# Optimization experiments

Measured on AMD Instinct MI355X. Metric: run time of the kernel, lower is better.

## Reference

```python
import jax, jax.numpy as jnp
import numpy as np

B, N, E = 64, 512, 262144
D_EMB = 128   # 2 * embedding_dim
D_H = 128     # residue_emb_dim == iegmn_lay_hid_dim
L = 5         # iegmn_n_lays
X_INIT = 0.25 # residual mix toward original coords (IEGMN x_connection_init)


def silu(x):
    return x * jax.nn.sigmoid(x)


def _edges(k):
    # within-graph random edges: pick a graph, then a node inside it
    g = jax.random.randint(k, (E,), 0, B)
    n = jax.random.randint(jax.random.fold_in(k, 1), (E,), 0, N)
    return (g * N + n).astype(jnp.int32)


def setup_inputs() -> dict:
    key = jax.random.key(0)
    ks = jax.random.split(key, 16)
    Nt = B * N
    s = 0.05
    feat = jax.random.normal(ks[0], (Nt, D_EMB), jnp.float32)
    coords = jax.random.normal(ks[1], (Nt, 3), jnp.float32)
    c_valid = (jax.random.uniform(ks[2], (B, N)) > 0.3).astype(jnp.float32)
    c_valid = c_valid.at[:, 0].set(1.0)  # avoid empty graphs
    return {
        'feat': feat,
        'coords': coords,
        'c_valid': c_valid,
        'edge_src': _edges(ks[3]), 'edge_dst': _edges(ks[4]),
        'cross_src': _edges(ks[5]), 'cross_dst': _edges(ks[6]),
        'W_emb': jax.random.normal(ks[7], (D_H, D_EMB), jnp.float32) * s,
        'We1': jax.random.normal(ks[8], (L, 2 * D_H + 1, D_H), jnp.float32) * s,
        'be1': jnp.zeros((L, D_H), jnp.float32),
        'We2': jax.random.normal(ks[9], (L, D_H, D_H), jnp.float32) * s,
        'be2': jnp.zeros((L, D_H), jnp.float32),
        'Wx': jax.random.normal(ks[10], (L, D_H, 1), jnp.float32) * s,
        'Wh': jax.random.normal(ks[11], (L, 3 * D_H, D_H), jnp.float32) * s,
        'bh': jnp.zeros((L, D_H), jnp.float32),
        'Wfc': jax.random.normal(ks[12], (3, D_H, D_H), jnp.float32) * s,
        'bfc': jnp.zeros((3, D_H), jnp.float32),
        'Wout': jax.random.normal(ks[13], (D_H, 1), jnp.float32) * s,
        'bout': jnp.zeros((1,), jnp.float32),
    }


def _deg_inv(dst, n):
    deg = jax.ops.segment_sum(jnp.ones(dst.shape[0], jnp.float32), dst, num_segments=n)
    return (1.0 / jnp.maximum(deg, 1.0))[:, None]


def _iegmn_layer(p, src, dst, x, h, x0, h0, deg_inv):
    We1, be1, We2, be2, Wx, Wh, bh = p
    n = x.shape[0]
    dx = x[src] - x[dst]                                  # [E, 3]
    d2 = jnp.sum(dx * dx, -1, keepdims=True)              # [E, 1]
    m = silu(jnp.concatenate([h[src], h[dst], d2], -1) @ We1 + be1)
    m = silu(m @ We2 + be2)                               # [E, D_H]
    coef = jnp.tanh(m @ Wx)                               # [E, 1]
    agg_x = jax.ops.segment_sum(dx * coef, dst, num_segments=n) * deg_inv
    x_new = X_INIT * x0 + (1.0 - X_INIT) * x + agg_x
    agg_m = jax.ops.segment_sum(m, dst, num_segments=n) * deg_inv
    h_new = silu(jnp.concatenate([h, agg_m, h0], -1) @ Wh + bh)
    return x_new, h_new


def reference(feat, coords, c_valid, edge_src, edge_dst, cross_src, cross_dst,
              W_emb, We1, be1, We2, be2, Wx, Wh, bh, Wfc, bfc, Wout, bout):
    Nt = feat.shape[0]
    h = feat @ W_emb.T          # embede (no bias)
    h0, x0, x = h, coords, coords
    dgi = _deg_inv(edge_dst, Nt)
    dci = _deg_inv(cross_dst, Nt)
    for k in range(L):
        p = tuple(t[k] for t in (We1, be1, We2, be2, Wx, Wh, bh))
        # branch == 'both': run layer on graph then cross_graph with same input h
        x, c1 = _iegmn_layer(p, edge_src, edge_dst, x, h, x0, h0, dgi)
        x, c2 = _iegmn_layer(p, cross_src, cross_dst, x, h, x0, h0, dci)
        h = c2 - c1             # dropout is identity at inference
    # masked sum-pool / count
    hb = h.reshape(B, N, D_H)
    pooled = jnp.sum(hb * c_valid[..., None], axis=1) / jnp.sum(c_valid, axis=1, keepdims=True)
    z = pooled
    for i in range(Wfc.shape[0]):
        z = jax.nn.relu(z @ Wfc[i] + bfc[i])
    out = jax.nn.sigmoid(z @ Wout + bout)
    return out.reshape(-1)      # [B]
```

## Files before the change

### kernel.cpp

```cpp
#include <hip/hip_runtime.h>

#define DEVINL __device__ __forceinline__

constexpr int NT   = 32768;
constexpr int DH   = 128;
constexpr int NE   = 262144;
constexpr int BGR  = 64;
constexpr int NPG  = 512;
constexpr int LAYS = 5;

typedef __attribute__((ext_vector_type(8))) short bf16x8;
typedef __attribute__((ext_vector_type(4))) float f32x4;
typedef __attribute__((ext_vector_type(4))) unsigned int uint4v;
typedef unsigned int uint;

DEVINL float siluf(float v){ return v * (1.0f/(1.0f + __expf(-v))); }
DEVINL float tanh_fast(float x){ float e = __expf(2.0f*x); return 1.0f - 2.0f/(e + 1.0f); }

DEVINL uint bf16_rne(float f){
  uint x = __float_as_uint(f);
  return (x + 0x7fffu + ((x>>16)&1u)) >> 16;
}

DEVINL void split8(const float* m, bf16x8& h, bf16x8& l){
  #pragma unroll
  for (int j=0;j<8;j++){
    uint x  = __float_as_uint(m[j]);
    uint hb = x >> 16;
    float hf = __uint_as_float(hb<<16);
    uint lb = bf16_rne(m[j] - hf);
    h[j] = (short)hb; l[j] = (short)lb;
  }
}

DEVINL f32x4 mma3(bf16x8 ah, bf16x8 al, bf16x8 bh, bf16x8 bl, f32x4 acc){
  acc = __builtin_amdgcn_mfma_f32_16x16x32_bf16(al, bh, acc, 0,0,0);
  acc = __builtin_amdgcn_mfma_f32_16x16x32_bf16(ah, bl, acc, 0,0,0);
  acc = __builtin_amdgcn_mfma_f32_16x16x32_bf16(ah, bh, acc, 0,0,0);
  return acc;
}

template<int TRANS>
__global__ __launch_bounds__(256) void k_prep(const float* __restrict__ src, short* __restrict__ dst){
  const int idx = blockIdx.x*256 + threadIdx.x;
  const int k = idx>>7, col = idx&127;
  const float v = TRANS ? src[(size_t)col*128 + k] : src[(size_t)k*128 + col];
  uint hb = __float_as_uint(v) >> 16;
  float hf = __uint_as_float(hb<<16);
  uint lb = bf16_rne(v - hf);
  const int kc = k>>5, q = (k&31)>>3, j = k&7;
  const size_t o = (size_t)kc*8192 + q*1024 + col*8 + j;
  dst[o]        = (short)hb;
  dst[o + 4096] = (short)lb;
}

__global__ __launch_bounds__(256) void k_hist(const int* __restrict__ dst, int* __restrict__ cnt){
  int e = blockIdx.x*256 + threadIdx.x;
  atomicAdd(&cnt[dst[e]], 1);
}

__global__ __launch_bounds__(1024) void k_scan(const int* __restrict__ cnt, int* __restrict__ cur){
  __shared__ int part[1024];
  const int tid = threadIdx.x;
  const int base = tid*32;
  int s = 0;
  for (int i=0;i<32;i++) s += cnt[base+i];
  const int own = s;
  part[tid] = s; __syncthreads();
  for (int off=1; off<1024; off<<=1){
    int v = (tid>=off) ? part[tid-off] : 0;
    __syncthreads();
    part[tid] += v;
    __syncthreads();
  }
  int run = part[tid] - own;
  for (int i=0;i<32;i++){ cur[base+i] = run; run += cnt[base+i]; }
}

__global__ __launch_bounds__(256) void k_invdeg(const int* __restrict__ cnt, float* __restrict__ dinv){
  int n = blockIdx.x*256 + threadIdx.x;
  int c = cnt[n];
  dinv[n] = 1.0f / (float)(c > 1 ? c : 1);
}

__global__ __launch_bounds__(256) void k_scatter(const int* __restrict__ dst, int* __restrict__ cur,
                                                 int* __restrict__ perm){
  int e = blockIdx.x*256 + threadIdx.x;
  int p = atomicAdd(&cur[dst[e]], 1);
  perm[p] = e;
}

template<int MODE>
__global__ __launch_bounds__(512) void k_ngemm(
    const float* __restrict__ A0, float* __restrict__ A1, const float* __restrict__ A2,
    const float* __restrict__ dinv, const short* __restrict__ W0, const short* __restrict__ W1,
    const float* __restrict__ bias, const float* __restrict__ c1in,
    float* __restrict__ out0, float* __restrict__ out1)
{
  __shared__ __align__(16) short wbuf[16384];
  const int tid = threadIdx.x;
  const int wv = tid>>6, lane = tid&63, c = lane&15, q = lane>>4;
  const int row = blockIdx.x*128 + wv*16 + c;
  float dv = 1.0f;
  if constexpr (MODE>=2) dv = dinv[row];
  f32x4 accA[8], accB[8];
  #pragma unroll
  for (int t=0;t<8;t++){
    #pragma unroll
    for (int r=0;r<4;r++){ accA[t][r]=0.f; if constexpr (MODE==1) accB[t][r]=0.f; }
  }
  const int fo = q*1024 + c*8;
  constexpr int NST = (MODE==1) ? 4 : ((MODE>=2) ? 6 : 2);
  for (int st=0; st<NST; ++st){
    __syncthreads();
    if constexpr (MODE==1){
      #pragma unroll
      for (int i=0;i<2;i++){
        ((uint4v*)wbuf)[tid + i*512]         = ((const uint4v*)(W0 + st*8192))[tid + i*512];
        ((uint4v*)(wbuf+8192))[tid + i*512]  = ((const uint4v*)(W1 + st*8192))[tid + i*512];
      }
    } else {
      #pragma unroll
      for (int i=0;i<4;i++)
        ((uint4v*)wbuf)[tid + i*512] = ((const uint4v*)(W0 + (size_t)st*16384))[tid + i*512];
    }
    __syncthreads();
    if constexpr (MODE==1){
      const int kb = st*32 + q*8;
      float4 v0 = *(const float4*)(A0 + (size_t)row*128 + kb);
      float4 v1 = *(const float4*)(A0 + (size_t)row*128 + kb + 4);
      float m[8] = {v0.x,v0.y,v0.z,v0.w,v1.x,v1.y,v1.z,v1.w};
      bf16x8 ah, al; split8(m, ah, al);
      #pragma unroll
      for (int t=0;t<8;t++){
        bf16x8 bhA = *(const bf16x8*)&wbuf[t*128 + fo];
        bf16x8 blA = *(const bf16x8*)&wbuf[4096 + t*128 + fo];
        bf16x8 bhB = *(const bf16x8*)&wbuf[8192 + t*128 + fo];
        bf16x8 blB = *(const bf16x8*)&wbuf[12288 + t*128 + fo];
        accA[t] = mma3(ah, al, bhA, blA, accA[t]);
        accB[t] = mma3(ah, al, bhB, blB, accB[t]);
      }
    } else {
      #pragma unroll
      for (int ks=0; ks<2; ++ks){
        const int kc = st*2 + ks;
        const float* asrc = A0; float sc = 1.0f; bool zero_a1 = false;
        if constexpr (MODE>=2){
          if (kc >= 8)      { asrc = A2; }
          else if (kc >= 4) { asrc = A1; sc = dv; zero_a1 = true; }
        }
        const int koff = (kc&3)*32 + q*8;
        float4 v0 = *(const float4*)(asrc + (size_t)row*128 + koff);
        float4 v1 = *(const float4*)(asrc + (size_t)row*128 + koff + 4);
        if constexpr (MODE>=2){
          if (zero_a1){
            float4 z; z.x=0.f; z.y=0.f; z.z=0.f; z.w=0.f;
            *(float4*)(A1 + (size_t)row*128 + koff)     = z;
            *(float4*)(A1 + (size_t)row*128 + koff + 4) = z;
          }
        }
        float m[8] = {v0.x*sc,v0.y*sc,v0.z*sc,v0.w*sc,v1.x*sc,v1.y*sc,v1.z*sc,v1.w*sc};
        bf16x8 ah, al; split8(m, ah, al);
        #pragma unroll
        for (int t=0;t<8;t++){
          bf16x8 bh = *(const bf16x8*)&wbuf[ks*8192 + t*128 + fo];
          bf16x8 bl = *(const bf16x8*)&wbuf[ks*8192 + 4096 + t*128 + fo];
          accA[t] = mma3(ah, al, bh, bl, accA[t]);
        }
      }
    }
  }
  #pragma unroll
  for (int t=0;t<8;t++){
    const int col = t*16 + c;
    float b0 = 0.f;
    if constexpr (MODE!=0) b0 = bias[col];
    #pragma unroll
    for (int r=0;r<4;r++){
      const size_t orow = (size_t)blockIdx.x*128 + wv*16 + q*4 + r;
      float v = accA[t][r];
      if constexpr (MODE==0){
        out0[orow*128 + col] = v; out1[orow*128 + col] = v;
      } else if constexpr (MODE==1){
        out0[orow*128 + col] = v + b0;
        out1[orow*128 + col] = accB[t][r];
      } else if constexpr (MODE==2){
        out0[orow*128 + col] = siluf(v + b0);
      } else {
        out0[orow*128 + col] = siluf(v + b0) - c1in[orow*128 + col];
      }
    }
  }
}

__global__ __launch_bounds__(512) void k_edge(
    const int* __restrict__ perm, const int* __restrict__ esrc, const int* __restrict__ edst,
    const float* __restrict__ x,  const float* __restrict__ Aw, const float* __restrict__ Bw,
    const short* __restrict__ w2p, const float* __restrict__ We1_l,
    const float* __restrict__ be2_l, const float* __restrict__ Wx_l,
    float* __restrict__ aggm, float* __restrict__ aggx)
{
  __shared__ __align__(16) short w2t[16384];
  __shared__ __align__(16) float w256s[128];
  __shared__ __align__(16) float wxs[128];
  __shared__ __align__(16) float be2s[128];
  __shared__ float dxs[128][3];
  __shared__ int   dsts[128];
  const int tid = threadIdx.x;
  const int wv = tid>>6, lane = tid&63, c = lane&15, q = lane>>4;
  if (tid < 128){ w256s[tid]=We1_l[256*128+tid]; wxs[tid]=Wx_l[tid]; be2s[tid]=be2_l[tid]; }
  const int er = wv*16 + c;
  const int eg = perm[blockIdx.x*128 + er];
  const int s  = esrc[eg], d = edst[eg];
  const float dx0 = x[s*3+0]-x[d*3+0];
  const float dx1 = x[s*3+1]-x[d*3+1];
  const float dx2 = x[s*3+2]-x[d*3+2];
  const float d2  = dx0*dx0 + dx1*dx1 + dx2*dx2;
  if (lane < 16){ dxs[er][0]=dx0; dxs[er][1]=dx1; dxs[er][2]=dx2; dsts[er]=d; }
  f32x4 acc[8];
  #pragma unroll
  for (int t=0;t<8;t++){ acc[t][0]=0.f; acc[t][1]=0.f; acc[t][2]=0.f; acc[t][3]=0.f; }
  const int fo = q*1024 + c*8;
  const float* ap = Aw + (size_t)s*128;
  const float* bp = Bw + (size_t)d*128;
  for (int half=0; half<2; ++half){
    __syncthreads();
    #pragma unroll
    for (int i=0;i<4;i++)
      ((uint4v*)w2t)[tid + i*512] = ((const uint4v*)(w2p + half*16384))[tid + i*512];
    __syncthreads();
    #pragma unroll
    for (int ks=0; ks<2; ++ks){
      const int kb = half*64 + ks*32 + q*8;
      float4 av0 = *(const float4*)(ap+kb), av1 = *(const float4*)(ap+kb+4);
      float4 bv0 = *(const float4*)(bp+kb), bv1 = *(const float4*)(bp+kb+4);
      float4 w0  = *(const float4*)&w256s[kb], w1 = *(const float4*)&w256s[kb+4];
      float m[8];
      m[0]=siluf(av0.x+bv0.x+d2*w0.x); m[1]=siluf(av0.y+bv0.y+d2*w0.y);
      m[2]=siluf(av0.z+bv0.z+d2*w0.z); m[3]=siluf(av0.w+bv0.w+d2*w0.w);
      m[4]=siluf(av1.x+bv1.x+d2*w1.x); m[5]=siluf(av1.y+bv1.y+d2*w1.y);
      m[6]=siluf(av1.z+bv1.z+d2*w1.z); m[7]=siluf(av1.w+bv1.w+d2*w1.w);
      bf16x8 ah, al; split8(m, ah, al);
      #pragma unroll
      for (int t=0;t<8;t++){
        bf16x8 bh = *(const bf16x8*)&w2t[ks*8192 + t*128 + fo];
        bf16x8 bl = *(const bf16x8*)&w2t[ks*8192 + 4096 + t*128 + fo];
        acc[t] = mma3(ah, al, bh, bl, acc[t]);
      }
    }
  }
  float pd[4];
  #pragma unroll
  for (int t=0;t<8;t++){
    const float be = be2s[t*16+c], wx = wxs[t*16+c];
    #pragma unroll
    for (int r=0;r<4;r++){
      float v = siluf(acc[t][r] + be);
      acc[t][r] = v;
      if (t==0) pd[r] = v*wx; else pd[r] += v*wx;
    }
  }
  #pragma unroll
  for (int msk=1; msk<16; msk<<=1){
    #pragma unroll
    for (int r=0;r<4;r++) pd[r] += __shfl_xor(pd[r], msk);
  }
  float coef[4];
  #pragma unroll
  for (int r=0;r<4;r++) coef[r] = tanh_fast(pd[r]);
  const int r0 = wv*16 + q*4;
  {
    int i = 0;
    while (i < 4){
      const int dd = dsts[r0+i];
      float sv[8];
      #pragma unroll
      for (int t=0;t<8;t++) sv[t] = acc[t][i];
      int i2 = i+1;
      while (i2 < 4 && dsts[r0+i2] == dd){
        #pragma unroll
        for (int t=0;t<8;t++) sv[t] += acc[t][i2];
        ++i2;
      }
      float* bm = aggm + (size_t)dd*128 + c;
      #pragma unroll
      for (int t=0;t<8;t++) unsafeAtomicAdd(bm + t*16, sv[t]);
      i = i2;
    }
  }
  if (c < 3){
    int i = 0;
    while (i < 4){
      const int dd = dsts[r0+i];
      float sv = dxs[r0+i][c]*coef[i];
      int i2 = i+1;
      while (i2 < 4 && dsts[r0+i2] == dd){ sv += dxs[r0+i2][c]*coef[i2]; ++i2; }
      unsafeAtomicAdd(aggx + (size_t)dd*3 + c, sv);
      i = i2;
    }
  }
}

__global__ __launch_bounds__(256) void k_xupd(float* __restrict__ x, const float* __restrict__ x0,
                                              float* __restrict__ aggx,
                                              const float* __restrict__ dinv){
  int i = blockIdx.x*256 + threadIdx.x;
  if (i < NT*3){
    int n = i/3;
    x[i] = 0.25f*x0[i] + 0.75f*x[i] + aggx[i]*dinv[n];
    aggx[i] = 0.f;
  }
}

__global__ __launch_bounds__(512) void k_pool(const float* __restrict__ h,
                                              const float* __restrict__ cvalid,
                                              float* __restrict__ pooled){
  __shared__ float red[4][128];
  __shared__ float redc[4];
  const int b = blockIdx.x, t = threadIdx.x, j = t&127, sl = t>>7;
  float s = 0.f, cf = 0.f;
  for (int n=sl; n<NPG; n+=4){
    const float m = cvalid[b*NPG + n];
    s  += h[((size_t)b*NPG + n)*DH + j] * m;
    cf += m;
  }
  red[sl][j] = s;
  if (j==0) redc[sl] = cf;
  __syncthreads();
  if (t < 128){
    float ss = red[0][t]+red[1][t]+red[2][t]+red[3][t];
    float cc = redc[0]+redc[1]+redc[2]+redc[3];
    pooled[b*DH + t] = ss / cc;
  }
}

__global__ __launch_bounds__(256) void k_mlp(const float* __restrict__ pooled,
                                             const float* __restrict__ Wfc,
                                             const float* __restrict__ bfc,
                                             const float* __restrict__ Wout,
                                             const float* __restrict__ bout,
                                             float* __restrict__ out)
{
  __shared__ __align__(16) float z[64*132];
  __shared__ __align__(16) float wB[128*128];
  const int t = threadIdx.x;
  {
    const int n = t>>2, qq = t&3;
    const float4* p = (const float4*)(pooled + n*DH + qq*32);
    float4* w = (float4*)&z[n*132 + qq*32];
    #pragma unroll
    for (int u=0;u<8;u++) w[u] = p[u];
  }
  const int g = t>>5, lane = t&31, c0 = lane*4;
  for (int l=0;l<3;l++){
    #pragma unroll
    for (int i=0;i<16;i++){
      const int idx = t + i*256;
      ((float4*)wB)[idx] = ((const float4*)(Wfc + (size_t)l*DH*DH))[idx];
    }
    __syncthreads();
    float acc[8][4];
    #pragma unroll
    for (int i=0;i<8;i++){ acc[i][0]=0.f; acc[i][1]=0.f; acc[i][2]=0.f; acc[i][3]=0.f; }
    #pragma unroll 4
    for (int kk=0; kk<128; kk+=4){
      float4 b0=*(const float4*)&wB[(kk+0)*128+c0];
      float4 b1=*(const float4*)&wB[(kk+1)*128+c0];
      float4 b2=*(const float4*)&wB[(kk+2)*128+c0];
      float4 b3=*(const float4*)&wB[(kk+3)*128+c0];
      #pragma unroll
      for (int i=0;i<8;i++){
        float4 a=*(const float4*)&z[(g*8+i)*132 + kk];
        acc[i][0]+=a.x*b0.x+a.y*b1.x+a.z*b2.x+a.w*b3.x;
        acc[i][1]+=a.x*b0.y+a.y*b1.y+a.z*b2.y+a.w*b3.y;
        acc[i][2]+=a.x*b0.z+a.y*b1.z+a.z*b2.z+a.w*b3.z;
        acc[i][3]+=a.x*b0.w+a.y*b1.w+a.z*b2.w+a.w*b3.w;
      }
    }
    __syncthreads();
    #pragma unroll
    for (int i=0;i<8;i++){
      float v0=acc[i][0]+bfc[l*DH+c0+0]; v0 = v0>0.f?v0:0.f;
      float v1=acc[i][1]+bfc[l*DH+c0+1]; v1 = v1>0.f?v1:0.f;
      float v2=acc[i][2]+bfc[l*DH+c0+2]; v2 = v2>0.f?v2:0.f;
      float v3=acc[i][3]+bfc[l*DH+c0+3]; v3 = v3>0.f?v3:0.f;
      float4 v; v.x=v0; v.y=v1; v.z=v2; v.w=v3;
      *(float4*)&z[(g*8+i)*132 + c0] = v;
    }
    __syncthreads();
  }
  if (t < 64){
    float a = 0.f;
    for (int k2=0;k2<128;k2++) a += z[t*132 + k2]*Wout[k2];
    out[t] = 1.0f/(1.0f + __expf(-(a + bout[0])));
  }
}

extern "C" void kernel_launch(void* const* d_in, const int* in_sizes, int n_in,
                              void* d_out, int out_size, void* d_ws, size_t ws_size,
                              hipStream_t stream)
{
  (void)in_sizes; (void)n_in; (void)out_size; (void)ws_size;
  const float* feat   = (const float*)d_in[0];
  const float* coords = (const float*)d_in[1];
  const float* cvalid = (const float*)d_in[2];
  const int*   esrc   = (const int*)d_in[3];
  const int*   edst   = (const int*)d_in[4];
  const int*   csrc   = (const int*)d_in[5];
  const int*   cdst   = (const int*)d_in[6];
  const float* W_emb  = (const float*)d_in[7];
  const float* We1    = (const float*)d_in[8];
  const float* be1    = (const float*)d_in[9];
  const float* We2    = (const float*)d_in[10];
  const float* be2    = (const float*)d_in[11];
  const float* Wx     = (const float*)d_in[12];
  const float* Wh     = (const float*)d_in[13];
  const float* bh     = (const float*)d_in[14];
  const float* Wfc    = (const float*)d_in[15];
  const float* bfc    = (const float*)d_in[16];
  const float* Wout   = (const float*)d_in[17];
  const float* bout   = (const float*)d_in[18];

  float* ws = (float*)d_ws;
  float* h      = ws; ws += (size_t)NT*DH;
  float* h0     = ws; ws += (size_t)NT*DH;
  float* c1     = ws; ws += (size_t)NT*DH;
  float* Aw     = ws; ws += (size_t)NT*DH;
  float* Bw     = ws; ws += (size_t)NT*DH;
  float* aggm   = ws; ws += (size_t)NT*DH;
  float* x      = ws; ws += (size_t)NT*3;
  float* aggx   = ws; ws += (size_t)NT*3;
  float* dgi    = ws; ws += NT;
  float* dci    = ws; ws += NT;
  float* pooled = ws; ws += BGR*DH;
  int* permG  = (int*)ws; ws += NE;
  int* permC  = (int*)ws; ws += NE;
  int* cnt    = (int*)ws; ws += NT;
  int* cursor = (int*)ws; ws += NT;
  short* pst    = (short*)ws;
  short* wemb_p = pst;
  const size_t LSTR = 32768*3 + 98304;
  short* lay_p  = pst + 32768;

  hipMemsetAsync(aggm, 0, (size_t)NT*DH*sizeof(float), stream);
  hipMemsetAsync(aggx, 0, (size_t)NT*3*sizeof(float), stream);

  k_prep<1><<<64, 256, 0, stream>>>(W_emb, wemb_p);
  for (int k=0;k<LAYS;k++){
    short* p = lay_p + (size_t)k*LSTR;
    k_prep<0><<<64,  256, 0, stream>>>(We1 + (size_t)k*257*DH,          p);
    k_prep<0><<<64,  256, 0, stream>>>(We1 + (size_t)k*257*DH + 128*DH, p + 32768);
    k_prep<0><<<64,  256, 0, stream>>>(We2 + (size_t)k*DH*DH,           p + 65536);
    k_prep<0><<<192, 256, 0, stream>>>(Wh  + (size_t)k*3*DH*DH,         p + 98304);
  }

  hipMemsetAsync(cnt, 0, NT*sizeof(int), stream);
  k_hist   <<<NE/256, 256, 0, stream>>>(edst, cnt);
  k_scan   <<<1, 1024, 0, stream>>>(cnt, cursor);
  k_invdeg <<<NT/256, 256, 0, stream>>>(cnt, dgi);
  k_scatter<<<NE/256, 256, 0, stream>>>(edst, cursor, permG);
  hipMemsetAsync(cnt, 0, NT*sizeof(int), stream);
  k_hist   <<<NE/256, 256, 0, stream>>>(cdst, cnt);
  k_scan   <<<1, 1024, 0, stream>>>(cnt, cursor);
  k_invdeg <<<NT/256, 256, 0, stream>>>(cnt, dci);
  k_scatter<<<NE/256, 256, 0, stream>>>(cdst, cursor, permC);

  k_ngemm<0><<<NT/128, 512, 0, stream>>>(feat, nullptr, nullptr, nullptr,
                                         wemb_p, nullptr, nullptr, nullptr, h, h0);
  hipMemcpyAsync(x, coords, (size_t)NT*3*sizeof(float), hipMemcpyDeviceToDevice, stream);

  for (int k=0; k<LAYS; k++){
    short* p = lay_p + (size_t)k*LSTR;
    const float* We1_l = We1 + (size_t)k*257*DH;
    const float* be1_l = be1 + (size_t)k*DH;
    const float* be2_l = be2 + (size_t)k*DH;
    const float* Wx_l  = Wx  + (size_t)k*DH;
    const float* bh_l  = bh  + (size_t)k*DH;

    k_ngemm<1><<<NT/128, 512, 0, stream>>>(h, nullptr, nullptr, nullptr,
                                           p, p + 32768, be1_l, nullptr, Aw, Bw);
    k_edge<<<NE/128, 512, 0, stream>>>(permG, esrc, edst, x, Aw, Bw,
                                       p + 65536, We1_l, be2_l, Wx_l, aggm, aggx);
    k_xupd<<<(NT*3+255)/256, 256, 0, stream>>>(x, coords, aggx, dgi);
    k_ngemm<2><<<NT/128, 512, 0, stream>>>(h, aggm, h0, dgi,
                                           p + 98304, nullptr, bh_l, nullptr, c1, nullptr);
    k_edge<<<NE/128, 512, 0, stream>>>(permC, csrc, cdst, x, Aw, Bw,
                                       p + 65536, We1_l, be2_l, Wx_l, aggm, aggx);
    k_xupd<<<(NT*3+255)/256, 256, 0, stream>>>(x, coords, aggx, dci);
    k_ngemm<3><<<NT/128, 512, 0, stream>>>(h, aggm, h0, dci,
                                           p + 98304, nullptr, bh_l, c1, h, nullptr);
  }

  k_pool<<<BGR, 512, 0, stream>>>(h, cvalid, pooled);
  k_mlp <<<1, 256, 0, stream>>>(pooled, Wfc, bfc, Wout, bout, (float*)d_out);
}
```

Baseline: 1.744 ms.

## Make edge kernel persistent over four tiles with fully resident W2 in LDS

The edge kernel now loads the whole 64KB split-bf16 We2 weight into shared memory once per block and loops over four 128-edge tiles. Before, it reloaded two halves of the weight for every 128-edge block. This amortizes the weight staging and the barriers across more edges, and the grid shrinks fourfold. The per-destination run merging for atomics is rewritten as a branchless suffix-sum with predicated atomics. The cost is larger LDS use per block, which lowers occupancy, and fewer blocks to fill the GPU.

```diff
diff --git a/kernel.cpp b/kernel.cpp
--- a/kernel.cpp
+++ b/kernel.cpp
@@ -8,6 +8,7 @@
 constexpr int BGR  = 64;
 constexpr int NPG  = 512;
 constexpr int LAYS = 5;
+constexpr int ETILES = 4;
 
 typedef __attribute__((ext_vector_type(8))) short bf16x8;
 typedef __attribute__((ext_vector_type(4))) float f32x4;
@@ -200,38 +201,39 @@
     const float* __restrict__ be2_l, const float* __restrict__ Wx_l,
     float* __restrict__ aggm, float* __restrict__ aggx)
 {
-  __shared__ __align__(16) short w2t[16384];
+  __shared__ __align__(16) short w2t[32768];
   __shared__ __align__(16) float w256s[128];
   __shared__ __align__(16) float wxs[128];
   __shared__ __align__(16) float be2s[128];
-  __shared__ float dxs[128][3];
-  __shared__ int   dsts[128];
+  __shared__ float dxs[8][16][3];
+  __shared__ int   dsts[8][16];
   const int tid = threadIdx.x;
   const int wv = tid>>6, lane = tid&63, c = lane&15, q = lane>>4;
   if (tid < 128){ w256s[tid]=We1_l[256*128+tid]; wxs[tid]=Wx_l[tid]; be2s[tid]=be2_l[tid]; }
-  const int er = wv*16 + c;
-  const int eg = perm[blockIdx.x*128 + er];
-  const int s  = esrc[eg], d = edst[eg];
-  const float dx0 = x[s*3+0]-x[d*3+0];
-  const float dx1 = x[s*3+1]-x[d*3+1];
-  const float dx2 = x[s*3+2]-x[d*3+2];
-  const float d2  = dx0*dx0 + dx1*dx1 + dx2*dx2;
-  if (lane < 16){ dxs[er][0]=dx0; dxs[er][1]=dx1; dxs[er][2]=dx2; dsts[er]=d; }
-  f32x4 acc[8];
   #pragma unroll
-  for (int t=0;t<8;t++){ acc[t][0]=0.f; acc[t][1]=0.f; acc[t][2]=0.f; acc[t][3]=0.f; }
+  for (int i=0;i<8;i++)
+    ((uint4v*)w2t)[tid + i*512] = ((const uint4v*)w2p)[tid + i*512];
+  __syncthreads();
+
   const int fo = q*1024 + c*8;
-  const float* ap = Aw + (size_t)s*128;
-  const float* bp = Bw + (size_t)d*128;
-  for (int half=0; half<2; ++half){
-    __syncthreads();
-    #pragma unroll
-    for (int i=0;i<4;i++)
-      ((uint4v*)w2t)[tid + i*512] = ((const uint4v*)(w2p + half*16384))[tid + i*512];
-    __syncthreads();
-    #pragma unroll
-    for (int ks=0; ks<2; ++ks){
-      const int kb = half*64 + ks*32 + q*8;
+  for (int tile=0; tile<ETILES; ++tile){
+    const int e0 = (blockIdx.x*ETILES + tile)*128;
+    const int er = wv*16 + c;
+    const int eg = perm[e0 + er];
+    const int s  = esrc[eg], d = edst[eg];
+    const float dx0 = x[s*3+0]-x[d*3+0];
+    const float dx1 = x[s*3+1]-x[d*3+1];
+    const float dx2 = x[s*3+2]-x[d*3+2];
+    const float d2  = dx0*dx0 + dx1*dx1 + dx2*dx2;
+    if (q==0){ dxs[wv][c][0]=dx0; dxs[wv][c][1]=dx1; dxs[wv][c][2]=dx2; dsts[wv][c]=d; }
+    f32x4 acc[8];
+    #pragma unroll
+    for (int t=0;t<8;t++){ acc[t][0]=0.f; acc[t][1]=0.f; acc[t][2]=0.f; acc[t][3]=0.f; }
+    const float* ap = Aw + (size_t)s*128;
+    const float* bp = Bw + (size_t)d*128;
+    #pragma unroll
+    for (int kc=0; kc<4; ++kc){
+      const int kb = kc*32 + q*8;
       float4 av0 = *(const float4*)(ap+kb), av1 = *(const float4*)(ap+kb+4);
       float4 bv0 = *(const float4*)(bp+kb), bv1 = *(const float4*)(bp+kb+4);
       float4 w0  = *(const float4*)&w256s[kb], w1 = *(const float4*)&w256s[kb+4];
@@ -243,60 +245,58 @@
       bf16x8 ah, al; split8(m, ah, al);
       #pragma unroll
       for (int t=0;t<8;t++){
-        bf16x8 bh = *(const bf16x8*)&w2t[ks*8192 + t*128 + fo];
-        bf16x8 bl = *(const bf16x8*)&w2t[ks*8192 + 4096 + t*128 + fo];
+        bf16x8 bh = *(const bf16x8*)&w2t[kc*8192 + t*128 + fo];
+        bf16x8 bl = *(const bf16x8*)&w2t[kc*8192 + 4096 + t*128 + fo];
         acc[t] = mma3(ah, al, bh, bl, acc[t]);
       }
     }
-  }
-  float pd[4];
-  #pragma unroll
-  for (int t=0;t<8;t++){
-    const float be = be2s[t*16+c], wx = wxs[t*16+c];
-    #pragma unroll
-    for (int r=0;r<4;r++){
-      float v = siluf(acc[t][r] + be);
-      acc[t][r] = v;
-      if (t==0) pd[r] = v*wx; else pd[r] += v*wx;
-    }
-  }
-  #pragma unroll
-  for (int msk=1; msk<16; msk<<=1){
-    #pragma unroll
-    for (int r=0;r<4;r++) pd[r] += __shfl_xor(pd[r], msk);
-  }
-  float coef[4];
-  #pragma unroll
-  for (int r=0;r<4;r++) coef[r] = tanh_fast(pd[r]);
-  const int r0 = wv*16 + q*4;
-  {
-    int i = 0;
-    while (i < 4){
-      const int dd = dsts[r0+i];
-      float sv[8];
-      #pragma unroll
-      for (int t=0;t<8;t++) sv[t] = acc[t][i];
-      int i2 = i+1;
-      while (i2 < 4 && dsts[r0+i2] == dd){
-        #pragma unroll
-        for (int t=0;t<8;t++) sv[t] += acc[t][i2];
-        ++i2;
-      }
-      float* bm = aggm + (size_t)dd*128 + c;
-      #pragma unroll
-      for (int t=0;t<8;t++) unsafeAtomicAdd(bm + t*16, sv[t]);
-      i = i2;
-    }
-  }
-  if (c < 3){
-    int i = 0;
-    while (i < 4){
-      const int dd = dsts[r0+i];
-      float sv = dxs[r0+i][c]*coef[i];
-      int i2 = i+1;
-      while (i2 < 4 && dsts[r0+i2] == dd){ sv += dxs[r0+i2][c]*coef[i2]; ++i2; }
-      unsafeAtomicAdd(aggx + (size_t)dd*3 + c, sv);
-      i = i2;
+    float pd[4];
+    #pragma unroll
+    for (int t=0;t<8;t++){
+      const float be = be2s[t*16+c], wx = wxs[t*16+c];
+      #pragma unroll
+      for (int r=0;r<4;r++){
+        float v = siluf(acc[t][r] + be);
+        acc[t][r] = v;
+        if (t==0) pd[r] = v*wx; else pd[r] += v*wx;
+      }
+    }
+    #pragma unroll
+    for (int msk=1; msk<16; msk<<=1){
+      #pragma unroll
+      for (int r=0;r<4;r++) pd[r] += __shfl_xor(pd[r], msk);
+    }
+    const int rb = q*4;
+    const int rd0 = dsts[wv][rb+0], rd1 = dsts[wv][rb+1];
+    const int rd2 = dsts[wv][rb+2], rd3 = dsts[wv][rb+3];
+    const bool b1 = (rd1!=rd0), b2 = (rd2!=rd1), b3 = (rd3!=rd2);
+    {
+      #pragma unroll
+      for (int t=0;t<8;t++){
+        const int col = t*16 + c;
+        float v3 = acc[t][3];
+        float v2 = acc[t][2] + (b3 ? 0.f : v3);
+        float v1 = acc[t][1] + (b2 ? 0.f : v2);
+        float v0 = acc[t][0] + (b1 ? 0.f : v1);
+        unsafeAtomicAdd(aggm + (size_t)rd0*128 + col, v0);
+        if (b1) unsafeAtomicAdd(aggm + (size_t)rd1*128 + col, v1);
+        if (b2) unsafeAtomicAdd(aggm + (size_t)rd2*128 + col, v2);
+        if (b3) unsafeAtomicAdd(aggm + (size_t)rd3*128 + col, v3);
+      }
+    }
+    if (c < 3){
+      float a0 = dxs[wv][rb+0][c]*tanh_fast(pd[0]);
+      float a1 = dxs[wv][rb+1][c]*tanh_fast(pd[1]);
+      float a2 = dxs[wv][rb+2][c]*tanh_fast(pd[2]);
+      float a3 = dxs[wv][rb+3][c]*tanh_fast(pd[3]);
+      float v3 = a3;
+      float v2 = a2 + (b3 ? 0.f : v3);
+      float v1 = a1 + (b2 ? 0.f : v2);
+      float v0 = a0 + (b1 ? 0.f : v1);
+      unsafeAtomicAdd(aggx + (size_t)rd0*3 + c, v0);
+      if (b1) unsafeAtomicAdd(aggx + (size_t)rd1*3 + c, v1);
+      if (b2) unsafeAtomicAdd(aggx + (size_t)rd2*3 + c, v2);
+      if (b3) unsafeAtomicAdd(aggx + (size_t)rd3*3 + c, v3);
     }
   }
 }
@@ -479,12 +479,12 @@
 
     k_ngemm<1><<<NT/128, 512, 0, stream>>>(h, nullptr, nullptr, nullptr,
                                            p, p + 32768, be1_l, nullptr, Aw, Bw);
-    k_edge<<<NE/128, 512, 0, stream>>>(permG, esrc, edst, x, Aw, Bw,
+    k_edge<<<NE/(128*ETILES), 512, 0, stream>>>(permG, esrc, edst, x, Aw, Bw,
                                        p + 65536, We1_l, be2_l, Wx_l, aggm, aggx);
     k_xupd<<<(NT*3+255)/256, 256, 0, stream>>>(x, coords, aggx, dgi);
     k_ngemm<2><<<NT/128, 512, 0, stream>>>(h, aggm, h0, dgi,
                                            p + 98304, nullptr, bh_l, nullptr, c1, nullptr);
-    k_edge<<<NE/128, 512, 0, stream>>>(permC, csrc, cdst, x, Aw, Bw,
+    k_edge<<<NE/(128*ETILES), 512, 0, stream>>>(permC, csrc, cdst, x, Aw, Bw,
                                        p + 65536, We1_l, be2_l, Wx_l, aggm, aggx);
     k_xupd<<<(NT*3+255)/256, 256, 0, stream>>>(x, coords, aggx, dci);
     k_ngemm<3><<<NT/128, 512, 0, stream>>>(h, aggm, h0, dci,
```

Result: slower. 2.836 ms (+62.6%).
